# Kernel optimization log

Measured on AMD Instinct MI355X. Metric: run time of the kernel, lower is better.

## Reference

```python
import jax, jax.numpy as jnp
import numpy as np
from jax import lax

TAU = 2.0
V_TH = 1.0
SG_ALPHA = 4.0  # spikingjelly default sigmoid surrogate alpha


def lif_multistep(x):
    """Multi-step LIF with hard reset to 0, v_init=0, detach_reset=True.
    x: (T, ...). Returns binary spikes (same shape), with sigmoid surrogate
    gradient injected via straight-through estimator.
    """
    def step(v, xt):
        h = v + (xt - v) / TAU                      # membrane charge
        s_hard = (h >= V_TH).astype(h.dtype)        # heaviside spike
        sur = jax.nn.sigmoid(SG_ALPHA * (h - V_TH))  # surrogate for grad
        s = s_hard + (sur - lax.stop_gradient(sur))  # fwd=hard, bwd=surrogate
        v_next = h * (1.0 - lax.stop_gradient(s))    # hard reset, detached
        return v_next, s
    _, spikes = lax.scan(step, jnp.zeros_like(x[0]), x)
    return spikes


def setup_inputs() -> dict:
    key = jax.random.key(0)
    ks = jax.random.split(key, 6)
    T, B, N, D = 4, 16, 197, 512
    w_std = 1.0 / np.sqrt(D)
    return {
        "x":  jax.random.normal(ks[0], (T, B, N, D), dtype=jnp.float32),
        "Wq": jax.random.normal(ks[1], (D, D), dtype=jnp.float32) * w_std,
        "Wk": jax.random.normal(ks[2], (D, D), dtype=jnp.float32) * w_std,
        "Wv": jax.random.normal(ks[3], (D, D), dtype=jnp.float32) * w_std,
        "Wp": jax.random.normal(ks[4], (D, D), dtype=jnp.float32) * w_std,
        "bp": jnp.zeros((D,), dtype=jnp.float32),
    }


def reference(x, Wq, Wk, Wv, Wp, bp):
    T, B, N, D = x.shape
    H = 8
    dh = D // H
    scale = dh ** -0.5

    # QKV projections (nn.Linear: x @ W.T, no bias)
    q = jnp.einsum('tbnd,ed->tbne', x, Wq)
    k = jnp.einsum('tbnd,ed->tbne', x, Wk)
    v = jnp.einsum('tbnd,ed->tbne', x, Wv)

    # LIF spiking over timestep dim T -> binary spike tensors
    qs = lif_multistep(q).reshape(T, B, N, H, dh).transpose(0, 1, 3, 2, 4)
    ks_ = lif_multistep(k).reshape(T, B, N, H, dh).transpose(0, 1, 3, 2, 4)
    vs = lif_multistep(v).reshape(T, B, N, H, dh).transpose(0, 1, 3, 2, 4)

    # spike-driven attention: binary matmul, no softmax
    attn = jnp.einsum('tbhnd,tbhmd->tbhnm', qs, ks_) * scale  # (T,B,H,N,N)
    attn_map = lax.stop_gradient(attn)
    out = jnp.einsum('tbhnm,tbhmd->tbhnd', attn, vs)          # (T,B,H,N,dh)
    out = out.transpose(0, 1, 3, 2, 4).reshape(T, B, N, D)

    # output projection + LIF
    out = jnp.einsum('tbnd,ed->tbne', out, Wp) + bp
    out = lif_multistep(out)
    return out, attn_map
```

## Files before the change

### kernel.cpp

```cpp
#include <hip/hip_runtime.h>
#include <stdint.h>

#define T_ 4
#define B_ 16
#define N_ 197
#define D_ 512
#define H_ 8
#define DH 64
#define BN_ (B_*N_)
#define PLANE (BN_*D_)
#define M_ (T_*BN_)
#define TENSOR_ELEMS (T_*PLANE)
#define WELEMS (D_*D_)
#define MH (M_*H_)
#define FLAG_TOL 6e-3f
#define NFW3 (3*PLANE/64)
#define NFWP (PLANE/64)

typedef __attribute__((ext_vector_type(8))) short short8v;
typedef __attribute__((ext_vector_type(8))) _Float16 f16x8;
typedef __attribute__((ext_vector_type(4))) float f32x4;
typedef __attribute__((ext_vector_type(16))) float f32x16;
typedef __attribute__((ext_vector_type(4))) unsigned short ushort4v;
typedef unsigned long long u64;
typedef unsigned int u32;

__device__ __forceinline__ ushort f16_bits(float f) {
    _Float16 h = (_Float16)f;
    return __builtin_bit_cast(unsigned short, h);
}
__device__ __forceinline__ float f16_val(ushort u) {
    return (float)__builtin_bit_cast(_Float16, u);
}

__device__ __forceinline__ void gload16(const void* g, void* l) {
    __builtin_amdgcn_global_load_lds(
        (const __attribute__((address_space(1))) unsigned int*)g,
        (__attribute__((address_space(3))) unsigned int*)l, 16, 0, 0);
}

__device__ __forceinline__ short8v unpack8(u32 bits) {
    short8v r;
    #pragma unroll
    for (int j = 0; j < 8; ++j)
        r[j] = (short)(((bits >> j) & 1u) ? 0x3F80 : 0);
    return r;
}

#define NBX (TENSOR_ELEMS/1024)
#define NBW (WELEMS/1024)

__global__ void cvt_all(const float* __restrict__ x,  const float* __restrict__ Wq,
                        const float* __restrict__ Wk, const float* __restrict__ Wv,
                        const float* __restrict__ Wp,
                        ushort* __restrict__ xh, ushort* __restrict__ w3h,
                        ushort* __restrict__ wph)
{
    int b = blockIdx.x;
    const float* src; ushort* dst; int base;
    if      (b < NBX)         { src = x;  dst = xh;             base = b; }
    else if (b < NBX + NBW)   { src = Wq; dst = w3h;            base = b - NBX; }
    else if (b < NBX + 2*NBW) { src = Wk; dst = w3h + WELEMS;   base = b - NBX - NBW; }
    else if (b < NBX + 3*NBW) { src = Wv; dst = w3h + 2*WELEMS; base = b - NBX - 2*NBW; }
    else                      { src = Wp; dst = wph;            base = b - NBX - 3*NBW; }
    int i = (base*256 + threadIdx.x)*4;
    float4 v = *(const float4*)(src + i);
    ushort4v o;
    o[0] = f16_bits(v.x); o[1] = f16_bits(v.y);
    o[2] = f16_bits(v.z); o[3] = f16_bits(v.w);
    *(ushort4v*)(dst + i) = o;
}

__global__ __launch_bounds__(256, 4)
void gemm_qkv_lif(const ushort* __restrict__ xh, const ushort* __restrict__ w3h,
                  u64* __restrict__ bits3, u64* __restrict__ fmap3)
{
    __shared__ __align__(16) ushort smem[16384];
    const int tid = threadIdx.x;
    const int lane = tid & 63, wn = tid >> 6;
    const int l31 = lane & 31, lg = lane >> 5;
    const int nyz = 12, nz = 3;

    int nwg = gridDim.x, orig = blockIdx.x;
    int q8 = nwg >> 3, r8 = nwg & 7, xcd = orig & 7, loc = orig >> 3;
    int wg = (xcd < r8 ? xcd*(q8+1) : r8*(q8+1) + (xcd-r8)*q8) + loc;
    int bx = wg / nyz, yz = wg - bx*nyz;
    int by = yz / nz,  z  = yz - by*nz;

    const int bm0 = bx * 32;
    const int bn0 = by * 128;
    const ushort* Wz = w3h + (size_t)z * WELEMS;

    f32x16 acc[4];
    #pragma unroll
    for (int t = 0; t < 4; ++t)
        #pragma unroll
        for (int r = 0; r < 16; ++r) acc[t][r] = 0.f;

    auto STAGE = [&](int buf, int kt) {
        #pragma unroll
        for (int i = 0; i < 4; ++i) {
            const int q = ((i & 1) << 8) | tid;
            const int row = q & 127, c = q >> 7;
            ushort* dst = smem + buf*8192 + ((i >> 1) << 12) + q*8;
            if (i < 2) {
                int t = row >> 5, r32 = row & 31;
                if (bm0 + r32 < BN_)
                    gload16(xh + ((size_t)(t*BN_ + bm0 + r32)*D_ + kt + c*8), dst);
            } else {
                gload16(Wz + ((size_t)(bn0 + row)*D_ + kt + c*8), dst);
            }
        }
    };
    auto COMPUTE = [&](int buf) {
        const ushort* base = smem + buf*8192;
        #pragma unroll
        for (int s = 0; s < 2; ++s) {
            const int cA = (s << 1) | lg;
            f16x8 bv = *(const f16x8*)&base[4096 + (cA*128 + wn*32 + l31)*8];
            #pragma unroll
            for (int t = 0; t < 4; ++t) {
                f16x8 av = *(const f16x8*)&base[(cA*128 + t*32 + l31)*8];
                acc[t] = __builtin_amdgcn_mfma_f32_32x32x16_f16(av, bv, acc[t], 0, 0, 0);
            }
        }
    };

    STAGE(0, 0);
    __syncthreads();
    int cur = 0;
    #pragma unroll
    for (int k32 = 0; k32 < 16; ++k32) {
        if (k32 < 15) STAGE(cur ^ 1, (k32 + 1)*32);
        COMPUTE(cur);
        __syncthreads();
        cur ^= 1;
    }

    u32* sp = (u32*)smem;
    u32* fl = (u32*)smem + 512;
    #pragma unroll
    for (int r = 0; r < 16; ++r) {
        bool s[4]; bool fg = false; float v = 0.f;
        #pragma unroll
        for (int t = 0; t < 4; ++t) {
            float h = v + (acc[t][r] - v)*0.5f;
            s[t] = h >= 1.0f;
            fg |= fabsf(h - 1.0f) < FLAG_TOL;
            v = s[t] ? 0.f : h;
        }
        #pragma unroll
        for (int t = 0; t < 4; ++t) {
            u64 m = __ballot(s[t]);
            if (lane == 0) {
                sp[((wn*4 + t)*16 + r)*2 + 0] = (u32)m;
                sp[((wn*4 + t)*16 + r)*2 + 1] = (u32)(m >> 32);
            }
        }
        u64 fm = __ballot(fg);
        if (lane == 0) {
            fl[(wn*16 + r)*2 + 0] = (u32)fm;
            fl[(wn*16 + r)*2 + 1] = (u32)(fm >> 32);
        }
    }
    __syncthreads();
    {
        int t = tid >> 6, row32 = (tid >> 1) & 31, hl = tid & 1;
        int rr = (row32 & 3) | ((row32 >> 3) << 2);
        int lgg = (row32 >> 2) & 1;
        u64 word = (u64)sp[(((2*hl)*4 + t)*16 + rr)*2 + lgg]
                 | ((u64)sp[(((2*hl+1)*4 + t)*16 + rr)*2 + lgg] << 32);
        if (bm0 + row32 < BN_)
            bits3[(size_t)z*MH + (size_t)(t*BN_ + bm0 + row32)*H_ + (bn0 >> 6) + hl] = word;
        if (tid < 64) {
            int rowf = tid >> 1, hlf = tid & 1;
            int rf = (rowf & 3) | ((rowf >> 3) << 2);
            int lgf = (rowf >> 2) & 1;
            u64 fw = (u64)fl[((2*hlf)*16 + rf)*2 + lgf]
                   | ((u64)fl[((2*hlf+1)*16 + rf)*2 + lgf] << 32);
            if (bm0 + rowf < BN_)
                fmap3[(size_t)z*NFWP + (size_t)(bm0 + rowf)*8 + (bn0 >> 6) + hlf] = fw;
        }
    }
}

__global__ __launch_bounds__(256, 4)
void gemm_proj_lif(const ushort* __restrict__ oh, const ushort* __restrict__ wph,
                   const float* __restrict__ bias, float* __restrict__ outp,
                   u64* __restrict__ fmapp)
{
    __shared__ __align__(16) ushort smem[16384];
    const int tid = threadIdx.x;
    const int lane = tid & 63, wn = tid >> 6;
    const int l31 = lane & 31, lg = lane >> 5;
    const int nyz = 4;

    int nwg = gridDim.x, orig = blockIdx.x;
    int q8 = nwg >> 3, r8 = nwg & 7, xcd = orig & 7, loc = orig >> 3;
    int wg = (xcd < r8 ? xcd*(q8+1) : r8*(q8+1) + (xcd-r8)*q8) + loc;
    int bx = wg / nyz, by = wg - bx*nyz;

    const int bm0 = bx * 32, bn0 = by * 128;

    f32x16 acc[4];
    #pragma unroll
    for (int t = 0; t < 4; ++t)
        #pragma unroll
        for (int r = 0; r < 16; ++r) acc[t][r] = 0.f;

    auto STAGE = [&](int buf, int kt) {
        #pragma unroll
        for (int i = 0; i < 4; ++i) {
            const int q = ((i & 1) << 8) | tid;
            const int row = q & 127, c = q >> 7;
            ushort* dst = smem + buf*8192 + ((i >> 1) << 12) + q*8;
            if (i < 2) {
                int t = row >> 5, r32 = row & 31;
                if (bm0 + r32 < BN_)
                    gload16(oh + ((size_t)(t*BN_ + bm0 + r32)*D_ + kt + c*8), dst);
            } else {
                gload16(wph + ((size_t)(bn0 + row)*D_ + kt + c*8), dst);
            }
        }
    };
    auto COMPUTE = [&](int buf) {
        const ushort* base = smem + buf*8192;
        #pragma unroll
        for (int s = 0; s < 2; ++s) {
            const int cA = (s << 1) | lg;
            f16x8 bv = *(const f16x8*)&base[4096 + (cA*128 + wn*32 + l31)*8];
            #pragma unroll
            for (int t = 0; t < 4; ++t) {
                f16x8 av = *(const f16x8*)&base[(cA*128 + t*32 + l31)*8];
                acc[t] = __builtin_amdgcn_mfma_f32_32x32x16_f16(av, bv, acc[t], 0, 0, 0);
            }
        }
    };

    STAGE(0, 0);
    __syncthreads();
    int cur = 0;
    #pragma unroll
    for (int k32 = 0; k32 < 16; ++k32) {
        if (k32 < 15) STAGE(cur ^ 1, (k32 + 1)*32);
        COMPUTE(cur);
        __syncthreads();
        cur ^= 1;
    }

    const int gcol = bn0 + wn*32 + l31;
    const float bb = bias[gcol];
    u32* fl = (u32*)smem;
    #pragma unroll
    for (int r = 0; r < 16; ++r) {
        const int row32 = (r & 3) + 8*(r >> 2) + 4*lg;
        const bool live = bm0 + row32 < BN_;
        bool fg = false; float v = 0.f;
        #pragma unroll
        for (int t = 0; t < 4; ++t) {
            float h = v + ((acc[t][r] + bb) - v)*0.5f;
            bool st = h >= 1.0f;
            fg |= fabsf(h - 1.0f) < FLAG_TOL;
            if (live)
                outp[(size_t)t*PLANE + (size_t)(bm0 + row32)*D_ + gcol] = st ? 1.0f : 0.0f;
            v = st ? 0.f : h;
        }
        u64 fm = __ballot(fg);
        if (lane == 0) {
            fl[(wn*16 + r)*2 + 0] = (u32)fm;
            fl[(wn*16 + r)*2 + 1] = (u32)(fm >> 32);
        }
    }
    __syncthreads();
    if (tid < 64) {
        int rowf = tid >> 1, hlf = tid & 1;
        int rf = (rowf & 3) | ((rowf >> 3) << 2);
        int lgf = (rowf >> 2) & 1;
        u64 fw = (u64)fl[((2*hlf)*16 + rf)*2 + lgf]
               | ((u64)fl[((2*hlf+1)*16 + rf)*2 + lgf] << 32);
        if (bm0 + rowf < BN_)
            fmapp[(size_t)(bm0 + rowf)*8 + (bn0 >> 6) + hlf] = fw;
    }
}

__global__ __launch_bounds__(256)
void fixup_qkv(const float* __restrict__ x,
               const float* __restrict__ Wq, const float* __restrict__ Wk,
               const float* __restrict__ Wv,
               u64* __restrict__ bits3, const u64* __restrict__ flagmap)
{
    const int lane = threadIdx.x & 63;
    const int wv = blockIdx.x*4 + (threadIdx.x >> 6);
    const int nw = gridDim.x*4;
    for (int w = wv; w < NFW3; w += nw) {
        u64 fm = flagmap[w];
        while (fm) {
            int bit = __ffsll((long long)fm) - 1;
            fm &= fm - 1;
            int id = (w << 6) + bit;
            int tsr = id / PLANE;
            int rem = id - tsr*PLANE;
            int r = rem >> 9, e = rem & (D_-1);
            const float* W = (tsr==0) ? Wq : (tsr==1 ? Wk : Wv);
            const float* wr = W + (size_t)e*D_;
            u64* bits = bits3 + (size_t)tsr*MH;
            float wv8[8];
            #pragma unroll
            for (int i = 0; i < 8; ++i) wv8[i] = wr[lane + 64*i];
            double dots[T_];
            #pragma unroll
            for (int t = 0; t < T_; ++t) {
                const float* xr = x + (size_t)(t*BN_ + r)*D_;
                float xv8[8];
                #pragma unroll
                for (int i = 0; i < 8; ++i) xv8[i] = xr[lane + 64*i];
                double p = 0.0;
                #pragma unroll
                for (int i = 0; i < 8; ++i) p += (double)xv8[i]*(double)wv8[i];
                dots[t] = p;
            }
            #pragma unroll
            for (int off = 32; off > 0; off >>= 1)
                #pragma unroll
                for (int t = 0; t < T_; ++t)
                    dots[t] += __shfl_down(dots[t], off);
            if (lane == 0) {
                double v = 0.0;
                u64 b = 1ull << (e & 63);
                #pragma unroll
                for (int t = 0; t < T_; ++t) {
                    double hh = v + (dots[t] - v)/2.0;
                    bool s = hh >= 1.0;
                    size_t wd = (size_t)(t*BN_ + r)*H_ + (e >> 6);
                    if (s) atomicOr(&bits[wd], b);
                    else   atomicAnd(&bits[wd], ~b);
                    v = s ? 0.0 : hh;
                }
            }
        }
    }
}

#define JP 224
#define VSTR 232

__global__ __launch_bounds__(256)
void attn_fused(const u64* __restrict__ qbits, const u64* __restrict__ kbits,
                const u64* __restrict__ vbits,
                float* __restrict__ attn_out, ushort* __restrict__ of16)
{
    __shared__ ushort Vt[DH][VSTR];
    __shared__ ushort Ss[4][16][VSTR];
    int tb = blockIdx.x, h = blockIdx.y;
    int tid = threadIdx.x, wave = tid >> 6, lane = tid & 63;

    for (int idx = tid; idx < JP*16; idx += 256) {
        int j = idx >> 4, d4 = (idx & 15) << 2;
        ushort vv[4] = {0,0,0,0};
        if (j < N_) {
            u64 vw = vbits[((size_t)tb*N_ + j)*H_ + h];
            #pragma unroll
            for (int r = 0; r < 4; ++r)
                vv[r] = ((vw >> (d4+r)) & 1ull) ? 0x3F80 : 0;
        }
        Vt[d4+0][j]=vv[0]; Vt[d4+1][j]=vv[1]; Vt[d4+2][j]=vv[2]; Vt[d4+3][j]=vv[3];
    }
    for (int idx = lane; idx < 16*16; idx += 64)
        Ss[wave][idx >> 4][208 + (idx & 15)] = 0;
    __syncthreads();

    const int il = lane & 15, kk = (lane >> 4) << 3, ig = (lane >> 4) << 2;
    const size_t amap = ((size_t)tb*H_ + h)*(size_t)(N_*N_);

    for (int it = wave; it < 13; it += 4) {
        int i0 = it << 4;
        int qrow = i0 + il;
        u64 qw = (qrow < N_) ? qbits[((size_t)tb*N_ + qrow)*H_ + h] : 0ull;
        short8v a0 = unpack8((u32)(qw >> kk));
        short8v a1 = unpack8((u32)((qw >> 32) >> kk));
        for (int jt = 0; jt < 13; ++jt) {
            int j0 = jt << 4, jrow = j0 + il;
            u64 kw = (jrow < N_) ? kbits[((size_t)tb*N_ + jrow)*H_ + h] : 0ull;
            short8v b0 = unpack8((u32)(kw >> kk));
            short8v b1 = unpack8((u32)((kw >> 32) >> kk));
            f32x4 c = {0.f, 0.f, 0.f, 0.f};
            c = __builtin_amdgcn_mfma_f32_16x16x32_bf16(a0, b0, c, 0, 0, 0);
            c = __builtin_amdgcn_mfma_f32_16x16x32_bf16(a1, b1, c, 0, 0, 0);
            int j = j0 + il;
            #pragma unroll
            for (int r = 0; r < 4; ++r) {
                float sv = c[r]*0.125f;
                Ss[wave][ig + r][j] = (ushort)(__float_as_uint(sv) >> 16);
            }
        }
        #pragma unroll
        for (int r = 0; r < 16; ++r) {
            int i = i0 + r;
            if (i < N_) {
                #pragma unroll
                for (int g = 0; g < 4; ++g) {
                    int col = g*64 + lane;
                    if (col < N_)
                        attn_out[amap + (size_t)i*N_ + col] =
                            __uint_as_float((u32)Ss[wave][r][col] << 16);
                }
            }
        }
        f32x4 o[4];
        #pragma unroll
        for (int dt = 0; dt < 4; ++dt) o[dt] = (f32x4){0.f,0.f,0.f,0.f};
        #pragma unroll
        for (int kt = 0; kt < 7; ++kt) {
            short8v a = *(const short8v*)&Ss[wave][il][kt*32 + kk];
            #pragma unroll
            for (int dt = 0; dt < 4; ++dt) {
                short8v b = *(const short8v*)&Vt[dt*16 + il][kt*32 + kk];
                o[dt] = __builtin_amdgcn_mfma_f32_16x16x32_bf16(a, b, o[dt], 0, 0, 0);
            }
        }
        #pragma unroll
        for (int dt = 0; dt < 4; ++dt)
            #pragma unroll
            for (int r = 0; r < 4; ++r) {
                int i = i0 + ig + r;
                if (i < N_)
                    of16[((size_t)tb*N_ + i)*D_ + (size_t)h*DH + dt*16 + il] =
                        f16_bits(o[dt][r]);
            }
    }
}

__global__ __launch_bounds__(256)
void fixup_proj(const ushort* __restrict__ of16, const float* __restrict__ Wp,
                const float* __restrict__ bp, float* __restrict__ outp,
                const u64* __restrict__ flagmap)
{
    const int lane = threadIdx.x & 63;
    const int wv = blockIdx.x*4 + (threadIdx.x >> 6);
    const int nw = gridDim.x*4;
    for (int w = wv; w < NFWP; w += nw) {
        u64 fm = flagmap[w];
        while (fm) {
            int bit = __ffsll((long long)fm) - 1;
            fm &= fm - 1;
            int rem = (w << 6) + bit;
            int r = rem >> 9, e = rem & (D_-1);
            const float* wr = Wp + (size_t)e*D_;
            float wv8[8];
            #pragma unroll
            for (int i = 0; i < 8; ++i) wv8[i] = wr[lane + 64*i];
            double dots[T_];
            #pragma unroll
            for (int t = 0; t < T_; ++t) {
                const ushort* ar = of16 + (size_t)(t*BN_ + r)*D_;
                float av8[8];
                #pragma unroll
                for (int i = 0; i < 8; ++i) av8[i] = f16_val(ar[lane + 64*i]);
                double p = 0.0;
                #pragma unroll
                for (int i = 0; i < 8; ++i) p += (double)av8[i]*(double)wv8[i];
                dots[t] = p;
            }
            #pragma unroll
            for (int off = 32; off > 0; off >>= 1)
                #pragma unroll
                for (int t = 0; t < T_; ++t)
                    dots[t] += __shfl_down(dots[t], off);
            if (lane == 0) {
                double v = 0.0;
                #pragma unroll
                for (int t = 0; t < T_; ++t) {
                    double xt = dots[t] + (double)bp[e];
                    double h = v + (xt - v)/2.0;
                    bool s = h >= 1.0;
                    outp[(size_t)t*PLANE + rem] = s ? 1.0f : 0.0f;
                    v = s ? 0.0 : h;
                }
            }
        }
    }
}

extern "C" void kernel_launch(void* const* d_in, const int* in_sizes, int n_in,
                              void* d_out, int out_size, void* d_ws, size_t ws_size,
                              hipStream_t stream)
{
    const float* x  = (const float*)d_in[0];
    const float* Wq = (const float*)d_in[1];
    const float* Wk = (const float*)d_in[2];
    const float* Wv = (const float*)d_in[3];
    const float* Wp = (const float*)d_in[4];
    const float* bp = (const float*)d_in[5];
    float* out_spk  = (float*)d_out;
    float* attn_out = (float*)d_out + TENSOR_ELEMS;

    char* ws = (char*)d_ws;
    const size_t BUFB = (size_t)TENSOR_ELEMS * sizeof(float);
    if (ws_size < 4*BUFB) return;
    ushort* of16 = (ushort*)(ws + 2*BUFB);
    char* r3 = ws + 3*BUFB;
    ushort* xh   = (ushort*)r3;
    ushort* w3h  = (ushort*)(r3 + (13u<<20));
    ushort* wph  = (ushort*)(r3 + (15u<<20));
    u64*    bits3 = (u64*)(r3 + (16u<<20));
    u64*    qbits = bits3;
    u64*    kbits = bits3 + MH;
    u64*    vbits = bits3 + 2*(size_t)MH;
    u64*    fmap3 = (u64*)(r3 + (19u<<20));
    u64*    fmapp = (u64*)(r3 + (20u<<20));

    cvt_all<<<NBX + 4*NBW, 256, 0, stream>>>(x, Wq, Wk, Wv, Wp, xh, w3h, wph);

    gemm_qkv_lif<<<99*12, 256, 0, stream>>>(xh, w3h, bits3, fmap3);
    fixup_qkv<<<2048, 256, 0, stream>>>(x, Wq, Wk, Wv, bits3, fmap3);

    attn_fused<<<dim3(T_*B_, H_), 256, 0, stream>>>(
        qbits, kbits, vbits, attn_out, of16);

    gemm_proj_lif<<<99*4, 256, 0, stream>>>(of16, wph, bp, out_spk, fmapp);
    fixup_proj<<<1024, 256, 0, stream>>>(of16, Wp, bp, out_spk, fmapp);
}
```

Before: 159.7 us.

## Pipeline GEMM loads with vmcnt waits and split attention rows across blocks

In both GEMM kernels the out-of-range row loads are now clamped to the last valid row instead of skipped, so every thread issues a fixed number of loads. That fixed count lets the loop wait on partial vmcnt(4) with raw s_barrier instead of a full __syncthreads, so the next tile's loads overlap the current MFMA work. The attention kernel launches twice as many blocks (grid z=2), each handling about half the query-row tiles, to raise occupancy. The cost is that each attention block rebuilds the full V tile, and the hand-written waitcnt depends on how gload16 is implemented.

New measurement: 165.1 us. 1.03x slower.

```diff
diff --git a/kernel.cpp b/kernel.cpp
--- a/kernel.cpp
+++ b/kernel.cpp
@@ -105,8 +105,8 @@
             ushort* dst = smem + buf*8192 + ((i >> 1) << 12) + q*8;
             if (i < 2) {
                 int t = row >> 5, r32 = row & 31;
-                if (bm0 + r32 < BN_)
-                    gload16(xh + ((size_t)(t*BN_ + bm0 + r32)*D_ + kt + c*8), dst);
+                int gr = bm0 + r32; if (gr > BN_-1) gr = BN_-1;
+                gload16(xh + ((size_t)(t*BN_ + gr)*D_ + kt + c*8), dst);
             } else {
                 gload16(Wz + ((size_t)(bn0 + row)*D_ + kt + c*8), dst);
             }
@@ -127,15 +127,22 @@
     };
 
     STAGE(0, 0);
+    int cur = 0;
+    #pragma unroll
+    for (int k32 = 0; k32 < 16; ++k32) {
+        if (k32 < 15) {
+            STAGE(cur ^ 1, (k32 + 1)*32);
+            asm volatile("s_waitcnt vmcnt(4)" ::: "memory");
+        } else {
+            asm volatile("s_waitcnt vmcnt(0)" ::: "memory");
+        }
+        __builtin_amdgcn_s_barrier();
+        __builtin_amdgcn_sched_barrier(0);
+        COMPUTE(cur);
+        __builtin_amdgcn_s_barrier();
+        cur ^= 1;
+    }
     __syncthreads();
-    int cur = 0;
-    #pragma unroll
-    for (int k32 = 0; k32 < 16; ++k32) {
-        if (k32 < 15) STAGE(cur ^ 1, (k32 + 1)*32);
-        COMPUTE(cur);
-        __syncthreads();
-        cur ^= 1;
-    }
 
     u32* sp = (u32*)smem;
     u32* fl = (u32*)smem + 512;
@@ -216,8 +223,8 @@
             ushort* dst = smem + buf*8192 + ((i >> 1) << 12) + q*8;
             if (i < 2) {
                 int t = row >> 5, r32 = row & 31;
-                if (bm0 + r32 < BN_)
-                    gload16(oh + ((size_t)(t*BN_ + bm0 + r32)*D_ + kt + c*8), dst);
+                int gr = bm0 + r32; if (gr > BN_-1) gr = BN_-1;
+                gload16(oh + ((size_t)(t*BN_ + gr)*D_ + kt + c*8), dst);
             } else {
                 gload16(wph + ((size_t)(bn0 + row)*D_ + kt + c*8), dst);
             }
@@ -238,15 +245,22 @@
     };
 
     STAGE(0, 0);
+    int cur = 0;
+    #pragma unroll
+    for (int k32 = 0; k32 < 16; ++k32) {
+        if (k32 < 15) {
+            STAGE(cur ^ 1, (k32 + 1)*32);
+            asm volatile("s_waitcnt vmcnt(4)" ::: "memory");
+        } else {
+            asm volatile("s_waitcnt vmcnt(0)" ::: "memory");
+        }
+        __builtin_amdgcn_s_barrier();
+        __builtin_amdgcn_sched_barrier(0);
+        COMPUTE(cur);
+        __builtin_amdgcn_s_barrier();
+        cur ^= 1;
+    }
     __syncthreads();
-    int cur = 0;
-    #pragma unroll
-    for (int k32 = 0; k32 < 16; ++k32) {
-        if (k32 < 15) STAGE(cur ^ 1, (k32 + 1)*32);
-        COMPUTE(cur);
-        __syncthreads();
-        cur ^= 1;
-    }
 
     const int gcol = bn0 + wn*32 + l31;
     const float bb = bias[gcol];
@@ -351,7 +365,7 @@
 {
     __shared__ ushort Vt[DH][VSTR];
     __shared__ ushort Ss[4][16][VSTR];
-    int tb = blockIdx.x, h = blockIdx.y;
+    int tb = blockIdx.x, h = blockIdx.y, zh = blockIdx.z;
     int tid = threadIdx.x, wave = tid >> 6, lane = tid & 63;
 
     for (int idx = tid; idx < JP*16; idx += 256) {
@@ -372,7 +386,9 @@
     const int il = lane & 15, kk = (lane >> 4) << 3, ig = (lane >> 4) << 2;
     const size_t amap = ((size_t)tb*H_ + h)*(size_t)(N_*N_);
 
-    for (int it = wave; it < 13; it += 4) {
+    const int it_lo = zh*7 + wave;
+    const int it_hi = (zh*7 + 7 < 13) ? zh*7 + 7 : 13;
+    for (int it = it_lo; it < it_hi; it += 4) {
         int i0 = it << 4;
         int qrow = i0 + il;
         u64 qw = (qrow < N_) ? qbits[((size_t)tb*N_ + qrow)*H_ + h] : 0ull;
@@ -514,7 +530,7 @@
     gemm_qkv_lif<<<99*12, 256, 0, stream>>>(xh, w3h, bits3, fmap3);
     fixup_qkv<<<2048, 256, 0, stream>>>(x, Wq, Wk, Wv, bits3, fmap3);
 
-    attn_fused<<<dim3(T_*B_, H_), 256, 0, stream>>>(
+    attn_fused<<<dim3(T_*B_, H_, 2), 256, 0, stream>>>(
         qbits, kbits, vbits, attn_out, of16);
 
     gemm_proj_lif<<<99*4, 256, 0, stream>>>(of16, wph, bp, out_spk, fmapp);
```

## Switch GEMMs to 2x2 wave tiling with 16x16 MFMA and split attention rows

Applied to the files above, without the earlier changes.

Both LIF GEMM kernels now split the 128x128 tile across a 2x2 wave grid and use 16x16x32 f16 MFMAs, replacing the 32x32x16 layout. The A rows are staged interleaved with timestep so each lane holds all four timesteps of one element, which lets the LIF epilogue write bit words straight from ballots without the shared-memory transpose and extra barrier. Occupancy hint drops from 4 to 3 blocks per CU. The attention kernel gains a z dimension of 2 that splits the query-row tiles, doubling the grid for more parallelism at the cost of rebuilding the V transpose in each block.

Result: slower. 166.4 us (+4.2%).

```diff
diff --git a/kernel.cpp b/kernel.cpp
--- a/kernel.cpp
+++ b/kernel.cpp
@@ -20,7 +20,6 @@
 typedef __attribute__((ext_vector_type(8))) short short8v;
 typedef __attribute__((ext_vector_type(8))) _Float16 f16x8;
 typedef __attribute__((ext_vector_type(4))) float f32x4;
-typedef __attribute__((ext_vector_type(16))) float f32x16;
 typedef __attribute__((ext_vector_type(4))) unsigned short ushort4v;
 typedef unsigned long long u64;
 typedef unsigned int u32;
@@ -71,14 +70,15 @@
     *(ushort4v*)(dst + i) = o;
 }
 
-__global__ __launch_bounds__(256, 4)
+__global__ __launch_bounds__(256, 3)
 void gemm_qkv_lif(const ushort* __restrict__ xh, const ushort* __restrict__ w3h,
                   u64* __restrict__ bits3, u64* __restrict__ fmap3)
 {
     __shared__ __align__(16) ushort smem[16384];
     const int tid = threadIdx.x;
-    const int lane = tid & 63, wn = tid >> 6;
-    const int l31 = lane & 31, lg = lane >> 5;
+    const int lane = tid & 63, wid = tid >> 6;
+    const int wm = wid >> 1, wn = wid & 1;
+    const int il = lane & 15, g = lane >> 4;
     const int nyz = 12, nz = 3;
 
     int nwg = gridDim.x, orig = blockIdx.x;
@@ -91,39 +91,43 @@
     const int bn0 = by * 128;
     const ushort* Wz = w3h + (size_t)z * WELEMS;
 
-    f32x16 acc[4];
-    #pragma unroll
-    for (int t = 0; t < 4; ++t)
-        #pragma unroll
-        for (int r = 0; r < 16; ++r) acc[t][r] = 0.f;
+    f32x4 acc[4][4];
+    #pragma unroll
+    for (int i = 0; i < 4; ++i)
+        #pragma unroll
+        for (int j = 0; j < 4; ++j)
+            acc[i][j] = (f32x4){0.f, 0.f, 0.f, 0.f};
 
     auto STAGE = [&](int buf, int kt) {
         #pragma unroll
         for (int i = 0; i < 4; ++i) {
             const int q = ((i & 1) << 8) | tid;
-            const int row = q & 127, c = q >> 7;
+            const int c = q >> 7, lrow = q & 127;
             ushort* dst = smem + buf*8192 + ((i >> 1) << 12) + q*8;
             if (i < 2) {
-                int t = row >> 5, r32 = row & 31;
-                if (bm0 + r32 < BN_)
-                    gload16(xh + ((size_t)(t*BN_ + bm0 + r32)*D_ + kt + c*8), dst);
+                int row32 = lrow >> 2, t = lrow & 3;
+                int gr = bm0 + row32; if (gr > BN_-1) gr = BN_-1;
+                gload16(xh + ((size_t)(t*BN_ + gr)*D_ + kt + c*8), dst);
             } else {
-                gload16(Wz + ((size_t)(bn0 + row)*D_ + kt + c*8), dst);
+                gload16(Wz + ((size_t)(bn0 + lrow)*D_ + kt + c*8), dst);
             }
         }
     };
     auto COMPUTE = [&](int buf) {
-        const ushort* base = smem + buf*8192;
-        #pragma unroll
-        for (int s = 0; s < 2; ++s) {
-            const int cA = (s << 1) | lg;
-            f16x8 bv = *(const f16x8*)&base[4096 + (cA*128 + wn*32 + l31)*8];
-            #pragma unroll
-            for (int t = 0; t < 4; ++t) {
-                f16x8 av = *(const f16x8*)&base[(cA*128 + t*32 + l31)*8];
-                acc[t] = __builtin_amdgcn_mfma_f32_32x32x16_f16(av, bv, acc[t], 0, 0, 0);
-            }
-        }
+        const ushort* Ab = smem + buf*8192;
+        const ushort* Bb = Ab + 4096;
+        f16x8 a[4], b[4];
+        #pragma unroll
+        for (int i = 0; i < 4; ++i)
+            a[i] = *(const f16x8*)&Ab[(g*128 + wm*64 + i*16 + il)*8];
+        #pragma unroll
+        for (int j = 0; j < 4; ++j)
+            b[j] = *(const f16x8*)&Bb[(g*128 + wn*64 + j*16 + il)*8];
+        #pragma unroll
+        for (int i = 0; i < 4; ++i)
+            #pragma unroll
+            for (int j = 0; j < 4; ++j)
+                acc[i][j] = __builtin_amdgcn_mfma_f32_16x16x32_f16(a[i], b[j], acc[i][j], 0, 0, 0);
     };
 
     STAGE(0, 0);
@@ -137,62 +141,60 @@
         cur ^= 1;
     }
 
-    u32* sp = (u32*)smem;
-    u32* fl = (u32*)smem + 512;
-    #pragma unroll
-    for (int r = 0; r < 16; ++r) {
-        bool s[4]; bool fg = false; float v = 0.f;
+    #pragma unroll
+    for (int i = 0; i < 4; ++i) {
+        bool s[4][4]; bool fg[4];
+        #pragma unroll
+        for (int j = 0; j < 4; ++j) {
+            fg[j] = false; float v = 0.f;
+            #pragma unroll
+            for (int t = 0; t < 4; ++t) {
+                float h = v + (acc[i][j][t] - v)*0.5f;
+                s[j][t] = h >= 1.0f;
+                fg[j] |= fabsf(h - 1.0f) < FLAG_TOL;
+                v = s[j][t] ? 0.f : h;
+            }
+        }
         #pragma unroll
         for (int t = 0; t < 4; ++t) {
-            float h = v + (acc[t][r] - v)*0.5f;
-            s[t] = h >= 1.0f;
-            fg |= fabsf(h - 1.0f) < FLAG_TOL;
-            v = s[t] ? 0.f : h;
-        }
-        #pragma unroll
-        for (int t = 0; t < 4; ++t) {
-            u64 m = __ballot(s[t]);
-            if (lane == 0) {
-                sp[((wn*4 + t)*16 + r)*2 + 0] = (u32)m;
-                sp[((wn*4 + t)*16 + r)*2 + 1] = (u32)(m >> 32);
-            }
-        }
-        u64 fm = __ballot(fg);
-        if (lane == 0) {
-            fl[(wn*16 + r)*2 + 0] = (u32)fm;
-            fl[(wn*16 + r)*2 + 1] = (u32)(fm >> 32);
-        }
-    }
-    __syncthreads();
-    {
-        int t = tid >> 6, row32 = (tid >> 1) & 31, hl = tid & 1;
-        int rr = (row32 & 3) | ((row32 >> 3) << 2);
-        int lgg = (row32 >> 2) & 1;
-        u64 word = (u64)sp[(((2*hl)*4 + t)*16 + rr)*2 + lgg]
-                 | ((u64)sp[(((2*hl+1)*4 + t)*16 + rr)*2 + lgg] << 32);
-        if (bm0 + row32 < BN_)
-            bits3[(size_t)z*MH + (size_t)(t*BN_ + bm0 + row32)*H_ + (bn0 >> 6) + hl] = word;
-        if (tid < 64) {
-            int rowf = tid >> 1, hlf = tid & 1;
-            int rf = (rowf & 3) | ((rowf >> 3) << 2);
-            int lgf = (rowf >> 2) & 1;
-            u64 fw = (u64)fl[((2*hlf)*16 + rf)*2 + lgf]
-                   | ((u64)fl[((2*hlf+1)*16 + rf)*2 + lgf] << 32);
-            if (bm0 + rowf < BN_)
-                fmap3[(size_t)z*NFWP + (size_t)(bm0 + rowf)*8 + (bn0 >> 6) + hlf] = fw;
-        }
-    }
-}
-
-__global__ __launch_bounds__(256, 4)
+            u64 b0 = __ballot(s[0][t]), b1 = __ballot(s[1][t]);
+            u64 b2 = __ballot(s[2][t]), b3 = __ballot(s[3][t]);
+            if (lane < 4) {
+                int sh = lane*16;
+                u64 w = ((b0 >> sh) & 0xFFFFull)
+                      | (((b1 >> sh) & 0xFFFFull) << 16)
+                      | (((b2 >> sh) & 0xFFFFull) << 32)
+                      | (((b3 >> sh) & 0xFFFFull) << 48);
+                int row32 = bm0 + wm*16 + i*4 + lane;
+                if (row32 < BN_)
+                    bits3[(size_t)z*MH + (size_t)(t*BN_ + row32)*H_ + by*2 + wn] = w;
+            }
+        }
+        u64 f0 = __ballot(fg[0]), f1 = __ballot(fg[1]);
+        u64 f2 = __ballot(fg[2]), f3 = __ballot(fg[3]);
+        if (lane < 4) {
+            int sh = lane*16;
+            u64 w = ((f0 >> sh) & 0xFFFFull)
+                  | (((f1 >> sh) & 0xFFFFull) << 16)
+                  | (((f2 >> sh) & 0xFFFFull) << 32)
+                  | (((f3 >> sh) & 0xFFFFull) << 48);
+            int row32 = bm0 + wm*16 + i*4 + lane;
+            if (row32 < BN_)
+                fmap3[(size_t)z*NFWP + (size_t)row32*8 + by*2 + wn] = w;
+        }
+    }
+}
+
+__global__ __launch_bounds__(256, 3)
 void gemm_proj_lif(const ushort* __restrict__ oh, const ushort* __restrict__ wph,
                    const float* __restrict__ bias, float* __restrict__ outp,
                    u64* __restrict__ fmapp)
 {
     __shared__ __align__(16) ushort smem[16384];
     const int tid = threadIdx.x;
-    const int lane = tid & 63, wn = tid >> 6;
-    const int l31 = lane & 31, lg = lane >> 5;
+    const int lane = tid & 63, wid = tid >> 6;
+    const int wm = wid >> 1, wn = wid & 1;
+    const int il = lane & 15, g = lane >> 4;
     const int nyz = 4;
 
     int nwg = gridDim.x, orig = blockIdx.x;
@@ -202,39 +204,43 @@
 
     const int bm0 = bx * 32, bn0 = by * 128;
 
-    f32x16 acc[4];
-    #pragma unroll
-    for (int t = 0; t < 4; ++t)
-        #pragma unroll
-        for (int r = 0; r < 16; ++r) acc[t][r] = 0.f;
+    f32x4 acc[4][4];
+    #pragma unroll
+    for (int i = 0; i < 4; ++i)
+        #pragma unroll
+        for (int j = 0; j < 4; ++j)
+            acc[i][j] = (f32x4){0.f, 0.f, 0.f, 0.f};
 
     auto STAGE = [&](int buf, int kt) {
         #pragma unroll
         for (int i = 0; i < 4; ++i) {
             const int q = ((i & 1) << 8) | tid;
-            const int row = q & 127, c = q >> 7;
+            const int c = q >> 7, lrow = q & 127;
             ushort* dst = smem + buf*8192 + ((i >> 1) << 12) + q*8;
             if (i < 2) {
-                int t = row >> 5, r32 = row & 31;
-                if (bm0 + r32 < BN_)
-                    gload16(oh + ((size_t)(t*BN_ + bm0 + r32)*D_ + kt + c*8), dst);
+                int row32 = lrow >> 2, t = lrow & 3;
+                int gr = bm0 + row32; if (gr > BN_-1) gr = BN_-1;
+                gload16(oh + ((size_t)(t*BN_ + gr)*D_ + kt + c*8), dst);
             } else {
-                gload16(wph + ((size_t)(bn0 + row)*D_ + kt + c*8), dst);
+                gload16(wph + ((size_t)(bn0 + lrow)*D_ + kt + c*8), dst);
             }
         }
     };
     auto COMPUTE = [&](int buf) {
-        const ushort* base = smem + buf*8192;
-        #pragma unroll
-        for (int s = 0; s < 2; ++s) {
-            const int cA = (s << 1) | lg;
-            f16x8 bv = *(const f16x8*)&base[4096 + (cA*128 + wn*32 + l31)*8];
-            #pragma unroll
-            for (int t = 0; t < 4; ++t) {
-                f16x8 av = *(const f16x8*)&base[(cA*128 + t*32 + l31)*8];
-                acc[t] = __builtin_amdgcn_mfma_f32_32x32x16_f16(av, bv, acc[t], 0, 0, 0);
-            }
-        }
+        const ushort* Ab = smem + buf*8192;
+        const ushort* Bb = Ab + 4096;
+        f16x8 a[4], b[4];
+        #pragma unroll
+        for (int i = 0; i < 4; ++i)
+            a[i] = *(const f16x8*)&Ab[(g*128 + wm*64 + i*16 + il)*8];
+        #pragma unroll
+        for (int j = 0; j < 4; ++j)
+            b[j] = *(const f16x8*)&Bb[(g*128 + wn*64 + j*16 + il)*8];
+        #pragma unroll
+        for (int i = 0; i < 4; ++i)
+            #pragma unroll
+            for (int j = 0; j < 4; ++j)
+                acc[i][j] = __builtin_amdgcn_mfma_f32_16x16x32_f16(a[i], b[j], acc[i][j], 0, 0, 0);
     };
 
     STAGE(0, 0);
@@ -248,38 +254,42 @@
         cur ^= 1;
     }
 
-    const int gcol = bn0 + wn*32 + l31;
-    const float bb = bias[gcol];
-    u32* fl = (u32*)smem;
-    #pragma unroll
-    for (int r = 0; r < 16; ++r) {
-        const int row32 = (r & 3) + 8*(r >> 2) + 4*lg;
-        const bool live = bm0 + row32 < BN_;
-        bool fg = false; float v = 0.f;
-        #pragma unroll
-        for (int t = 0; t < 4; ++t) {
-            float h = v + ((acc[t][r] + bb) - v)*0.5f;
-            bool st = h >= 1.0f;
-            fg |= fabsf(h - 1.0f) < FLAG_TOL;
-            if (live)
-                outp[(size_t)t*PLANE + (size_t)(bm0 + row32)*D_ + gcol] = st ? 1.0f : 0.0f;
-            v = st ? 0.f : h;
-        }
-        u64 fm = __ballot(fg);
-        if (lane == 0) {
-            fl[(wn*16 + r)*2 + 0] = (u32)fm;
-            fl[(wn*16 + r)*2 + 1] = (u32)(fm >> 32);
-        }
-    }
-    __syncthreads();
-    if (tid < 64) {
-        int rowf = tid >> 1, hlf = tid & 1;
-        int rf = (rowf & 3) | ((rowf >> 3) << 2);
-        int lgf = (rowf >> 2) & 1;
-        u64 fw = (u64)fl[((2*hlf)*16 + rf)*2 + lgf]
-               | ((u64)fl[((2*hlf+1)*16 + rf)*2 + lgf] << 32);
-        if (bm0 + rowf < BN_)
-            fmapp[(size_t)(bm0 + rowf)*8 + (bn0 >> 6) + hlf] = fw;
+    const int colbase = bn0 + wn*64;
+    float bb[4];
+    #pragma unroll
+    for (int j = 0; j < 4; ++j) bb[j] = bias[colbase + j*16 + il];
+
+    #pragma unroll
+    for (int i = 0; i < 4; ++i) {
+        const int myrow = bm0 + wm*16 + i*4 + g;
+        const bool live = myrow < BN_;
+        bool fg[4];
+        #pragma unroll
+        for (int j = 0; j < 4; ++j) {
+            fg[j] = false; float v = 0.f;
+            #pragma unroll
+            for (int t = 0; t < 4; ++t) {
+                float h = v + ((acc[i][j][t] + bb[j]) - v)*0.5f;
+                bool st = h >= 1.0f;
+                fg[j] |= fabsf(h - 1.0f) < FLAG_TOL;
+                if (live)
+                    outp[(size_t)t*PLANE + (size_t)myrow*D_ + colbase + j*16 + il] =
+                        st ? 1.0f : 0.0f;
+                v = st ? 0.f : h;
+            }
+        }
+        u64 f0 = __ballot(fg[0]), f1 = __ballot(fg[1]);
+        u64 f2 = __ballot(fg[2]), f3 = __ballot(fg[3]);
+        if (lane < 4) {
+            int sh = lane*16;
+            u64 w = ((f0 >> sh) & 0xFFFFull)
+                  | (((f1 >> sh) & 0xFFFFull) << 16)
+                  | (((f2 >> sh) & 0xFFFFull) << 32)
+                  | (((f3 >> sh) & 0xFFFFull) << 48);
+            int row32 = bm0 + wm*16 + i*4 + lane;
+            if (row32 < BN_)
+                fmapp[(size_t)row32*8 + by*2 + wn] = w;
+        }
     }
 }
 
@@ -351,7 +361,7 @@
 {
     __shared__ ushort Vt[DH][VSTR];
     __shared__ ushort Ss[4][16][VSTR];
-    int tb = blockIdx.x, h = blockIdx.y;
+    int tb = blockIdx.x, h = blockIdx.y, zh = blockIdx.z;
     int tid = threadIdx.x, wave = tid >> 6, lane = tid & 63;
 
     for (int idx = tid; idx < JP*16; idx += 256) {
@@ -372,7 +382,9 @@
     const int il = lane & 15, kk = (lane >> 4) << 3, ig = (lane >> 4) << 2;
     const size_t amap = ((size_t)tb*H_ + h)*(size_t)(N_*N_);
 
-    for (int it = wave; it < 13; it += 4) {
+    const int it_lo = zh*7 + wave;
+    const int it_hi = (zh*7 + 7 < 13) ? zh*7 + 7 : 13;
+    for (int it = it_lo; it < it_hi; it += 4) {
         int i0 = it << 4;
         int qrow = i0 + il;
         u64 qw = (qrow < N_) ? qbits[((size_t)tb*N_ + qrow)*H_ + h] : 0ull;
@@ -398,8 +410,8 @@
             int i = i0 + r;
             if (i < N_) {
                 #pragma unroll
-                for (int g = 0; g < 4; ++g) {
-                    int col = g*64 + lane;
+                for (int gg = 0; gg < 4; ++gg) {
+                    int col = gg*64 + lane;
                     if (col < N_)
                         attn_out[amap + (size_t)i*N_ + col] =
                             __uint_as_float((u32)Ss[wave][r][col] << 16);
@@ -514,7 +526,7 @@
     gemm_qkv_lif<<<99*12, 256, 0, stream>>>(xh, w3h, bits3, fmap3);
     fixup_qkv<<<2048, 256, 0, stream>>>(x, Wq, Wk, Wv, bits3, fmap3);
 
-    attn_fused<<<dim3(T_*B_, H_), 256, 0, stream>>>(
+    attn_fused<<<dim3(T_*B_, H_, 2), 256, 0, stream>>>(
         qbits, kbits, vbits, attn_out, of16);
 
     gemm_proj_lif<<<99*4, 256, 0, stream>>>(of16, wph, bp, out_spk, fmapp);
```
